# Optimization experiments

Hardware: AMD Instinct MI355X
Metric: run time of the kernel (lower is better)

Reference implementation:

```python
import jax, jax.numpy as jnp
import numpy as np

B, T, D, H = 2, 2048, 1024, 16
DH = D // H
PD = 6
SCALE = DH ** -0.5
_PAIRS4 = [(0, 1), (0, 2), (0, 3), (1, 2), (1, 3), (2, 3)]
_J6 = jnp.array([[0, 0, 0, 0, 0, 1], [0, 0, 0, 0, -1, 0], [0, 0, 0, 1, 0, 0],
                 [0, 0, 1, 0, 0, 0], [0, -1, 0, 0, 0, 0], [1, 0, 0, 0, 0, 0]], dtype=jnp.float32)


def exterior(p1, p2):
    # p1, p2: (..., 4) -> normalized 6-d Plucker line (..., 6)
    parts = [p1[..., i] * p2[..., j] - p1[..., j] * p2[..., i] for i, j in _PAIRS4]
    L = jnp.stack(parts, axis=-1)
    n = jnp.linalg.norm(L, axis=-1, keepdims=True)
    return L / jnp.clip(n, 1e-12)


def setup_inputs() -> dict:
    key = jax.random.key(0)
    ks = jax.random.split(key, 12)
    s = 0.02
    return {
        'x': jax.random.normal(ks[0], (B, T, D), jnp.float32),
        'qkv_w': jax.random.normal(ks[1], (D, 3 * D), jnp.float32) * s,
        'qkv_b': jnp.zeros((3 * D,), jnp.float32),
        'w1_write': jax.random.normal(ks[2], (D, 4 * H), jnp.float32) * s,
        'w2_write': jax.random.normal(ks[3], (D, 4 * H), jnp.float32) * s,
        'w1_read': jax.random.normal(ks[4], (D, 4 * H), jnp.float32) * s,
        'w2_read': jax.random.normal(ks[5], (D, 4 * H), jnp.float32) * s,
        'memv_w': jax.random.normal(ks[6], (D, D), jnp.float32) * s,
        'memv_b': jnp.zeros((D,), jnp.float32),
        'memg_w': jax.random.normal(ks[7], (D, H), jnp.float32) * s,
        'memg_b': jnp.zeros((H,), jnp.float32),
        'mem_scale': jnp.full((H,), 0.1, jnp.float32),
        'rw_mix': jnp.zeros((), jnp.float32),
        'out_w': jax.random.normal(ks[8], (D, D), jnp.float32) * s,
        'out_b': jnp.zeros((D,), jnp.float32),
        'decay_logits': jnp.full((H,), 4.6, jnp.float32),
    }


def reference(x, qkv_w, qkv_b, w1_write, w2_write, w1_read, w2_read,
              memv_w, memv_b, memg_w, memg_b, mem_scale, rw_mix,
              out_w, out_b, decay_logits):
    # ---- standard causal softmax attention ----
    qkv = (x @ qkv_w + qkv_b).reshape(B, T, 3, H, DH).transpose(2, 0, 3, 1, 4)
    q, k, v = qkv[0], qkv[1], qkv[2]                      # each (B,H,T,DH)
    scores = jnp.einsum('bhtd,bhsd->bhts', q, k) * SCALE
    mask = jnp.triu(jnp.ones((T, T), bool), 1)
    scores = jnp.where(mask[None, None], -jnp.inf, scores)
    attn = jax.nn.softmax(scores, axis=-1)                # dropout=0 (eval)
    seq_out = jnp.einsum('bhts,bhsd->bthd', attn, v).reshape(B, T, D)

    # ---- Plucker lines for write (prev->cur) and read ----
    x_prev = jnp.concatenate([jnp.zeros((B, 1, D), x.dtype), x[:, :-1]], axis=1)
    w1 = (x_prev @ w1_write).reshape(B, T, H, 4)
    w2 = (x @ w2_write).reshape(B, T, H, 4)
    write_lines = exterior(w1, w2)                        # (B,T,H,6)
    r1 = (x @ w1_read).reshape(B, T, H, 4)
    r2 = (x @ w2_read).reshape(B, T, H, 4)
    read_lines = exterior(r1, r2)

    Jw = jnp.einsum('bthi,ij->bhtj', write_lines, _J6)    # (B,H,T,6)
    Jr = jnp.einsum('bthi,ij->bhtj', read_lines, _J6)
    rd = read_lines.transpose(0, 2, 1, 3)                 # (B,H,T,6)

    # ---- decay-weighted cumsum of 6x6 outer-product states ----
    decays = jax.nn.sigmoid(decay_logits)                 # (H,)
    pos = jnp.arange(T, dtype=x.dtype)
    decay_inv = (1.0 / jnp.clip(decays, 1e-6))[:, None] ** pos[None]   # (H,T)
    decay_fwd = decays[:, None] ** pos[None]                           # (H,T)

    def shifted_state(Jv):
        outer = Jv[..., :, None] * Jv[..., None, :]       # (B,H,T,6,6)
        ow = outer * decay_inv[None, :, :, None, None]
        M = jnp.cumsum(ow, axis=2)
        M = jnp.concatenate([jnp.zeros((B, H, 1, PD, PD), x.dtype), M[:, :, :-1]], axis=2)
        return M * decay_fwd[None, :, :, None, None]

    Mw = shifted_state(Jw)
    Mr = shifted_state(Jr)

    score_w = jnp.einsum('bhti,bhtij,bhtj->bht', rd, Mw, rd)
    score_r = jnp.einsum('bhti,bhtij,bhtj->bht', Jw, Mr, Jw)
    alpha = jax.nn.sigmoid(rw_mix)
    mem_score = (1 - alpha) * score_w + alpha * score_r   # (B,H,T)

    mem_val = x @ memv_w + memv_b                         # (B,T,D)
    gate = jax.nn.sigmoid(x @ memg_w + memg_b)            # (B,T,H)
    mem_score_t = mem_score.transpose(0, 2, 1)            # (B,T,H)
    gated = jax.nn.sigmoid(mem_score_t * mem_scale[None, None, :]) * gate
    gated = gated.mean(axis=-1, keepdims=True)            # (B,T,1)

    return (seq_out + gated * mem_val) @ out_w + out_b
```

## Files before the change

### kernel.cpp

```cpp
#include <hip/hip_runtime.h>

#define Bb 2
#define Tt 2048
#define Dd 1024
#define Hh 16
#define LDC 4480

typedef __attribute__((ext_vector_type(8))) short s16x8;
typedef __attribute__((ext_vector_type(4))) float f32x4;
typedef __attribute__((ext_vector_type(8))) _Float16 f16x8;

__device__ __forceinline__ float bf2f(unsigned short u) {
  unsigned v = ((unsigned)u) << 16;
  union { unsigned u; float f; } c; c.u = v; return c.f;
}
__device__ __forceinline__ unsigned short f2bf(float f) {
  union { float f; unsigned u; } c; c.f = f;
  unsigned u = c.u + 0x7fffu + ((c.u >> 16) & 1u);
  return (unsigned short)(u >> 16);
}
__device__ __forceinline__ float sigm(float x) { return 1.f / (1.f + expf(-x)); }

typedef const __attribute__((address_space(1))) void* gas_ptr;
typedef __attribute__((address_space(3))) void* las_ptr;
__device__ __forceinline__ void gload_lds16(const unsigned short* g, unsigned short* l) {
  __builtin_amdgcn_global_load_lds((gas_ptr)g, (las_ptr)l, 16, 0, 0);
}



__global__ __launch_bounds__(256) void prep_kernel(const float* __restrict__ x,
                                                   const float* __restrict__ qkv_w,
                                                   const float* __restrict__ w1w,
                                                   const float* __restrict__ w2w,
                                                   const float* __restrict__ w1r,
                                                   const float* __restrict__ w2r,
                                                   const float* __restrict__ memg_w,
                                                   const float* __restrict__ memv_w,
                                                   const float* __restrict__ out_w,
                                                   const float* __restrict__ qkv_b,
                                                   const float* __restrict__ memg_b,
                                                   const float* __restrict__ memv_b,
                                                   unsigned short* __restrict__ xb,
                                                   unsigned short* __restrict__ WT,
                                                   unsigned short* __restrict__ outT,
                                                   float* __restrict__ biasC) {
  __shared__ float tile[32][33];
  int id = blockIdx.x;
  if (id < 2048) {
    int i = id * 256 + threadIdx.x;
    int row = i >> 7;
    int k8 = i & 127;
    const float4* xv = reinterpret_cast<const float4*>(x + (size_t)i * 8);
    float4 a = xv[0], b = xv[1];
    s16x8 out;
    out[0] = (short)f2bf(a.x); out[1] = (short)f2bf(a.y);
    out[2] = (short)f2bf(a.z); out[3] = (short)f2bf(a.w);
    out[4] = (short)f2bf(b.x); out[5] = (short)f2bf(b.y);
    out[6] = (short)f2bf(b.z); out[7] = (short)f2bf(b.w);
    int mt = row >> 4, kt = k8 >> 2, quad = k8 & 3;
    int lane = (row & 15) + quad * 16;
    *(s16x8*)&xb[(((size_t)mt * 32 + kt) * 64 + lane) * 8] = out;
  } else if (id < 6528) {
    int j = id - 2048;
    int n0 = (j % 140) * 32, kt = j / 140, k0 = kt * 32;
    int tx = threadIdx.x & 31, ty = threadIdx.x >> 5;
#pragma unroll
    for (int i = 0; i < 4; i++) {
      int k = k0 + ty + i * 8, n = n0 + tx;
      float v;
      if (n < 3072)       v = qkv_w[(size_t)k * 3072 + n];
      else if (n < 3136)  v = w1w[k * 64 + (n - 3072)];
      else if (n < 3200)  v = w2w[k * 64 + (n - 3136)];
      else if (n < 3264)  v = w1r[k * 64 + (n - 3200)];
      else if (n < 3328)  v = w2r[k * 64 + (n - 3264)];
      else if (n < 3344)  v = memg_w[k * 16 + (n - 3328)];
      else if (n < 3392)  v = 0.f;
      else if (n < 4416)  v = memv_w[(size_t)k * 1024 + (n - 3392)];
      else                v = 0.f;
      tile[ty + i * 8][tx] = v;
    }
    __syncthreads();
    if (threadIdx.x < 128) {
      int nl = threadIdx.x & 31, quad = threadIdx.x >> 5;
      s16x8 out;
#pragma unroll
      for (int e = 0; e < 8; e++) out[e] = (short)f2bf(tile[quad * 8 + e][nl]);
      int nt = (n0 >> 4) + (nl >> 4);
      int lane = (nl & 15) + quad * 16;
      *(s16x8*)&WT[(((size_t)nt * 32 + kt) * 64 + lane) * 8] = out;
    }
  } else if (id < 7552) {
    int j = id - 6528;
    int n0 = (j & 31) * 32, kt = j >> 5, k0 = kt * 32;
    int tx = threadIdx.x & 31, ty = threadIdx.x >> 5;
#pragma unroll
    for (int i = 0; i < 4; i++) {
      int k = k0 + ty + i * 8, n = n0 + tx;
      tile[ty + i * 8][tx] = out_w[(size_t)k * 1024 + n];
    }
    __syncthreads();
    if (threadIdx.x < 128) {
      int nl = threadIdx.x & 31, quad = threadIdx.x >> 5;
      s16x8 out;
#pragma unroll
      for (int e = 0; e < 8; e++) out[e] = (short)f2bf(tile[quad * 8 + e][nl]);
      int nt = (n0 >> 4) + (nl >> 4);
      int lane = (nl & 15) + quad * 16;
      *(s16x8*)&outT[(((size_t)nt * 32 + kt) * 64 + lane) * 8] = out;
    }
  } else {
    int i = (id - 7552) * 256 + threadIdx.x;
    if (i < LDC) {
      float v = 0.f;
      if (i < 3072) v = qkv_b[i];
      else if (i >= 3328 && i < 3344) v = memg_b[i - 3328];
      else if (i >= 3392 && i < 4416) v = memv_b[i - 3392];
      biasC[i] = v;
    }
  }
}


template <int MODE>
__global__ __launch_bounds__(256) void gemm_frag_kernel(const unsigned short* __restrict__ Af,
                                                        const unsigned short* __restrict__ Bf,
                                                        void* __restrict__ Cout,
                                                        const float* __restrict__ bias) {
  __shared__ __align__(16) unsigned short lds[2][16][512];
  int mTile, nTile;
  if (MODE == 0) {
    const int xx = blockIdx.x & 7, local = blockIdx.x >> 3;
    mTile = (xx >> 1) * 8 + (local & 7);
    nTile = (xx & 1) * 18 + (local >> 3);
    if (nTile >= 35) return;
  } else {
    mTile = blockIdx.x >> 3;
    nTile = blockIdx.x & 7;
  }
  const int lane = threadIdx.x & 63, wid = threadIdx.x >> 6;
  const int quad = lane >> 4, c16 = lane & 15;
  const int wm = wid >> 1, wn = wid & 1;
  const int mt0 = mTile * 8 + wm * 4;
  const int nt0 = nTile * 8 + wn * 4;

  const unsigned short* src[4];
#pragma unroll
  for (int i = 0; i < 4; i++) {
    int f = wid * 4 + i;
    src[i] = ((f < 8) ? (Af + (size_t)(mTile * 8 + f) * 16384)
                      : (Bf + (size_t)(nTile * 8 + (f - 8)) * 16384))
             + (size_t)lane * 8;
  }

  f32x4 acc[4][4] = {};

#pragma unroll
  for (int i = 0; i < 4; i++) gload_lds16(src[i], &lds[0][wid * 4 + i][0]);
  __syncthreads();

  int buf = 0;
  for (int kt = 0; kt < 32; kt++) {
    if (kt + 1 < 32) {
#pragma unroll
      for (int i = 0; i < 4; i++)
        gload_lds16(src[i] + (size_t)(kt + 1) * 512, &lds[buf ^ 1][wid * 4 + i][0]);
    }
    s16x8 a[4], b[4];
#pragma unroll
    for (int i = 0; i < 4; i++) {
      a[i] = *(const s16x8*)&lds[buf][wm * 4 + i][lane * 8];
      b[i] = *(const s16x8*)&lds[buf][8 + wn * 4 + i][lane * 8];
    }
#pragma unroll
    for (int mt = 0; mt < 4; mt++)
#pragma unroll
      for (int nt = 0; nt < 4; nt++)
        acc[mt][nt] = __builtin_amdgcn_mfma_f32_16x16x32_bf16(a[mt], b[nt],
                                                              acc[mt][nt], 0, 0, 0);
    __syncthreads();
    buf ^= 1;
  }

#pragma unroll
  for (int mt = 0; mt < 4; mt++)
#pragma unroll
    for (int nt = 0; nt < 4; nt++) {
      int col = (nt0 + nt) * 16 + c16;
      float bv = bias[col];
#pragma unroll
      for (int r = 0; r < 4; r++) {
        int row = (mt0 + mt) * 16 + quad * 4 + r;
        if (MODE == 0)
          ((unsigned short*)Cout)[(size_t)row * 4480 + col] = f2bf(acc[mt][nt][r] + bv);
        else
          ((float*)Cout)[(size_t)row * 1024 + col] = acc[mt][nt][r] + bv;
      }
    }
}


__device__ __forceinline__ void ext6(const float* p, const float* q, float* L) {
  L[0] = p[0] * q[1] - p[1] * q[0];
  L[1] = p[0] * q[2] - p[2] * q[0];
  L[2] = p[0] * q[3] - p[3] * q[0];
  L[3] = p[1] * q[2] - p[2] * q[1];
  L[4] = p[1] * q[3] - p[3] * q[1];
  L[5] = p[2] * q[3] - p[3] * q[2];
  float n = sqrtf(L[0]*L[0] + L[1]*L[1] + L[2]*L[2] + L[3]*L[3] + L[4]*L[4] + L[5]*L[5]);
  float inv = 1.f / fmaxf(n, 1e-12f);
#pragma unroll
  for (int k = 0; k < 6; k++) L[k] *= inv;
}


__global__ __launch_bounds__(256) void post1_kernel(const unsigned short* __restrict__ Cq,
                                                    unsigned short* __restrict__ Kt,
                                                    unsigned short* __restrict__ Vt,
                                                    float* __restrict__ Jw,
                                                    float* __restrict__ Jr,
                                                    float* __restrict__ rd) {
  __shared__ unsigned short vt[32 * 66];
  int id = blockIdx.x;
  int tid = threadIdx.x;
  if (id < 2048) {
    int kb = id & 63, bh = id >> 6;
    int b = bh >> 4, h = bh & 15;
    size_t tbase = ((size_t)bh * 64 + kb) * 2048;
    {
      int key = tid >> 3, p = tid & 7, dg = p ^ (key & 7);
      size_t src = (size_t)(b * Tt + kb * 32 + key) * LDC + 1024 + h * 64 + dg * 8;
      s16x8 kv = *(const s16x8*)&Cq[src];
      *(s16x8*)&Kt[tbase + (size_t)tid * 8] = kv;
    }
    {
      int row = tid >> 3, c = tid & 7;
      size_t src = (size_t)(b * Tt + kb * 32 + row) * LDC + 2048 + h * 64 + c * 8;
      s16x8 vv = *(const s16x8*)&Cq[src];
#pragma unroll
      for (int e = 0; e < 8; e++) {
        union { _Float16 hf; unsigned short s; } cv;
        cv.hf = (_Float16)bf2f((unsigned short)vv[e]);
        vt[row * 66 + c * 8 + e] = cv.s;
      }
    }
    __syncthreads();
    {
      int d = tid >> 2, p = tid & 3, cq = p ^ ((d >> 2) & 3);
      s16x8 out;
#pragma unroll
      for (int e = 0; e < 8; e++) {
        int key = ((e >> 2) & 1) * 16 + cq * 4 + (e & 3);
        out[e] = (short)vt[key * 66 + d];
      }
      *(s16x8*)&Vt[tbase + (size_t)tid * 8] = out;
    }
  } else {
    int idx = (id - 2048) * 256 + tid;
    int h = idx & 15, t = (idx >> 4) & 2047, b = idx >> 15;
    size_t row = (size_t)(b * Tt + t) * LDC;
    float w1[4], w2[4], r1[4], r2[4];
#pragma unroll
    for (int k = 0; k < 4; k++) {
      w1[k] = (t > 0) ? bf2f(Cq[row - LDC + 3072 + h * 4 + k]) : 0.f;
      w2[k] = bf2f(Cq[row + 3136 + h * 4 + k]);
      r1[k] = bf2f(Cq[row + 3200 + h * 4 + k]);
      r2[k] = bf2f(Cq[row + 3264 + h * 4 + k]);
    }
    float Lw[6], Lr[6];
    ext6(w1, w2, Lw);
    ext6(r1, r2, Lr);
    size_t ob = ((size_t)(b * Hh + h) * Tt + t) * 6;
    Jw[ob + 0] = Lw[5]; Jw[ob + 1] = -Lw[4]; Jw[ob + 2] = Lw[3];
    Jw[ob + 3] = Lw[2]; Jw[ob + 4] = -Lw[1]; Jw[ob + 5] = Lw[0];
    Jr[ob + 0] = Lr[5]; Jr[ob + 1] = -Lr[4]; Jr[ob + 2] = Lr[3];
    Jr[ob + 3] = Lr[2]; Jr[ob + 4] = -Lr[1]; Jr[ob + 5] = Lr[0];
#pragma unroll
    for (int k = 0; k < 6; k++) rd[ob + k] = Lr[k];
  }
}


__device__ __forceinline__ void do_tile(int ks, int q0, int quad, int c16,
                                        const s16x8& qf0, const s16x8& qf1,
                                        const s16x8 kf[2][2], const f16x8 vb[4],
                                        float& l_i, f32x4 o[4]) {
  f32x4 st0 = {}, st1 = {};
  __builtin_amdgcn_s_setprio(1);
  st0 = __builtin_amdgcn_mfma_f32_16x16x32_bf16(kf[0][0], qf0, st0, 0, 0, 0);
  st0 = __builtin_amdgcn_mfma_f32_16x16x32_bf16(kf[0][1], qf1, st0, 0, 0, 0);
  st1 = __builtin_amdgcn_mfma_f32_16x16x32_bf16(kf[1][0], qf0, st1, 0, 0, 0);
  st1 = __builtin_amdgcn_mfma_f32_16x16x32_bf16(kf[1][1], qf1, st1, 0, 0, 0);
  __builtin_amdgcn_s_setprio(0);
  bool need_mask = (ks + 31 > q0);
  f16x8 pa;
  float lp = 0.f;
#pragma unroll
  for (int r = 0; r < 4; r++) {
    float v0 = st0[r] * 0.125f;
    float v1 = st1[r] * 0.125f;
    if (need_mask) {
      v0 = (ks + quad * 4 + r      <= q0 + c16) ? v0 : -1e30f;
      v1 = (ks + 16 + quad * 4 + r <= q0 + c16) ? v1 : -1e30f;
    }
    float p0 = __expf(v0);
    float p1 = __expf(v1);
    lp += p0 + p1;
    pa[r]     = (_Float16)p0;
    pa[4 + r] = (_Float16)p1;
  }
  l_i += lp;
  __builtin_amdgcn_s_setprio(1);
#pragma unroll
  for (int nt = 0; nt < 4; nt++)
    o[nt] = __builtin_amdgcn_mfma_f32_16x16x32_f16(pa, vb[nt], o[nt], 0, 0, 0);
  __builtin_amdgcn_s_setprio(0);
}

__global__ __launch_bounds__(256) void attn_kernel(const unsigned short* __restrict__ Cq,
                                                   const unsigned short* __restrict__ Kt,
                                                   const unsigned short* __restrict__ Vt,
                                                   unsigned short* __restrict__ po) {
  const int id = blockIdx.x;
  const int xcd = id & 7, rest = id >> 3;
  const int g = rest & 15;
  const int bh = ((rest >> 4) << 3) | xcd;
  const int b = bh >> 4, h = bh & 15;
  const int w = threadIdx.x >> 6, lane = threadIdx.x & 63;
  const int quad = lane >> 4, c16 = lane & 15;
  const int pi = g * 4 + w;
  const int qA = pi * 16, qB = 2032 - pi * 16;
  const int nkA = qA + 16, nkB = 2048 - pi * 16;
  const char* Kbase = (const char*)(Kt + (size_t)bh * 64 * 2048);
  const char* Vbase = (const char*)(Vt + (size_t)bh * 64 * 2048);
  const int vK0 = c16 * 128 + ((quad       ^ (c16 & 7)) * 16);
  const int vK1 = c16 * 128 + (((4 + quad) ^ (c16 & 7)) * 16);
  const int vV  = c16 * 64  + ((quad ^ ((c16 >> 2) & 3)) * 16);

  size_t rowA = (size_t)(b * Tt + qA + c16) * LDC + h * 64;
  size_t rowB = (size_t)(b * Tt + qB + c16) * LDC + h * 64;
  s16x8 qA0 = *(const s16x8*)&Cq[rowA + quad * 8];
  s16x8 qA1 = *(const s16x8*)&Cq[rowA + 32 + quad * 8];
  s16x8 qB0 = *(const s16x8*)&Cq[rowB + quad * 8];
  s16x8 qB1 = *(const s16x8*)&Cq[rowB + 32 + quad * 8];

  float lA = 0.f, lB = 0.f;
  f32x4 oA[4] = {}, oB[4] = {};

  s16x8 kfX[2][2], kfY[2][2];
  f16x8 vbX[4], vbY[4];

#define LOADT(dstK, dstV, kb) do {                                   \
    const char* Kb_ = Kbase + (size_t)(kb) * 4096;                   \
    const char* Vb_ = Vbase + (size_t)(kb) * 4096;                   \
    dstK[0][0] = *(const s16x8*)(Kb_ + vK0);                         \
    dstK[0][1] = *(const s16x8*)(Kb_ + vK1);                         \
    dstK[1][0] = *(const s16x8*)(Kb_ + 2048 + vK0);                  \
    dstK[1][1] = *(const s16x8*)(Kb_ + 2048 + vK1);                  \
    dstV[0] = *(const f16x8*)(Vb_ + vV);                             \
    dstV[1] = *(const f16x8*)(Vb_ + 1024 + vV);                      \
    dstV[2] = *(const f16x8*)(Vb_ + 2048 + vV);                      \
    dstV[3] = *(const f16x8*)(Vb_ + 3072 + vV);                      \
  } while (0)

  LOADT(kfX, vbX, 0);
  for (int ks = 0; ks < nkB; ks += 64) {
    if (ks + 32 < nkB) LOADT(kfY, vbY, (ks >> 5) + 1);
    do_tile(ks, qB, quad, c16, qB0, qB1, kfX, vbX, lB, oB);
    if (ks < nkA)
      do_tile(ks, qA, quad, c16, qA0, qA1, kfX, vbX, lA, oA);
    if (ks + 32 < nkB) {
      if (ks + 64 < nkB) LOADT(kfX, vbX, (ks >> 5) + 2);
      do_tile(ks + 32, qB, quad, c16, qB0, qB1, kfY, vbY, lB, oB);
      if (ks + 32 < nkA)
        do_tile(ks + 32, qA, quad, c16, qA0, qA1, kfY, vbY, lA, oA);
    }
  }
#undef LOADT

  lB += __shfl_xor(lB, 16, 64); lB += __shfl_xor(lB, 32, 64);
  lA += __shfl_xor(lA, 16, 64); lA += __shfl_xor(lA, 32, 64);
  float invB = 1.f / lB, invA = 1.f / lA;
#pragma unroll
  for (int r = 0; r < 4; r++) {
    float ivB = __shfl(invB, quad * 4 + r, 64);
    float ivA = __shfl(invA, quad * 4 + r, 64);
    size_t baseB = (size_t)(b * Tt + qB + quad * 4 + r) * Dd + h * 64;
    size_t baseA = (size_t)(b * Tt + qA + quad * 4 + r) * Dd + h * 64;
#pragma unroll
    for (int nt = 0; nt < 4; nt++) {
      po[baseB + nt * 16 + c16] = f2bf(oB[nt][r] * ivB);
      po[baseA + nt * 16 + c16] = f2bf(oA[nt][r] * ivA);
    }
  }
}


__global__ __launch_bounds__(64) void scanA_kernel(const float* __restrict__ Jw,
                                                   const float* __restrict__ Jr,
                                                   const float* __restrict__ decay_logits,
                                                   float* __restrict__ chunkA) {
  int blk = blockIdx.x;
  int chunk = blk & 15, bh = (blk >> 4) & 31, type = blk >> 9;
  int lane = threadIdx.x;
  const float* V = (type == 0 ? Jw : Jr) + ((size_t)bh * Tt + chunk * 128) * 6;
  __shared__ float v[768];
  for (int i = lane; i < 768; i += 64) v[i] = V[i];
  __syncthreads();
  float d = sigm(decay_logits[bh & 15]);
  int ll = lane < 36 ? lane : 35;
  int i6 = ll / 6, j6 = ll % 6;
  float A = 0.f;
  for (int s = 0; s < 128; s++) A = d * A + v[s * 6 + i6] * v[s * 6 + j6];
  if (lane < 36) chunkA[((size_t)(type * 32 + bh) * 16 + chunk) * 36 + lane] = A;
}


__global__ __launch_bounds__(128) void scanB_kernel(const float* __restrict__ Jw,
                                                    const float* __restrict__ Jr,
                                                    const float* __restrict__ rd,
                                                    const float* __restrict__ chunkA,
                                                    const float* __restrict__ decay_logits,
                                                    float* __restrict__ score_w,
                                                    float* __restrict__ score_r) {
  int blk = blockIdx.x;
  int chunk = blk & 15, bh = (blk >> 4) & 31, type = blk >> 9;
  int tl = threadIdx.x;
  size_t tb = ((size_t)bh * Tt + chunk * 128) * 6;
  const float* U = (type == 0 ? rd : Jw) + tb;
  const float* W = (type == 0 ? Jw : Jr) + tb;
  __shared__ float wv[768];
  __shared__ float Bm[36];
  for (int i = tl; i < 768; i += 128) wv[i] = W[i];
  float d = sigm(decay_logits[bh & 15]);
  if (tl < 36) {
    float dS = powf(d, 128.f);
    float Bv = 0.f;
    size_t base = (size_t)(type * 32 + bh) * 16;
    for (int c = 0; c < chunk; c++)
      Bv = dS * Bv + d * chunkA[(base + c) * 36 + tl];
    Bm[tl] = Bv;
  }
  __syncthreads();
  float u[6];
#pragma unroll
  for (int i = 0; i < 6; i++) u[i] = U[tl * 6 + i];
  float q = 0.f;
#pragma unroll
  for (int i = 0; i < 6; i++) {
    float bi = 0.f;
#pragma unroll
    for (int j = 0; j < 6; j++) bi += Bm[i * 6 + j] * u[j];
    q += u[i] * bi;
  }
  float acc = 0.f;
  for (int s = 0; s < tl; s++) {
    const float* ws = &wv[s * 6];
    float dot = u[0]*ws[0] + u[1]*ws[1] + u[2]*ws[2] + u[3]*ws[3] + u[4]*ws[4] + u[5]*ws[5];
    acc = d * (acc + dot * dot);
  }
  float score = acc + powf(d, (float)tl) * q;
  float* outp = (type == 0 ? score_w : score_r);
  outp[(size_t)bh * Tt + chunk * 128 + tl] = score;
}


__global__ __launch_bounds__(256) void combine_kernel(const unsigned short* __restrict__ po,
                                                      const unsigned short* __restrict__ Cq,
                                                      const float* __restrict__ score_w,
                                                      const float* __restrict__ score_r,
                                                      const float* __restrict__ mem_scale,
                                                      const float* __restrict__ rw_mix,
                                                      unsigned short* __restrict__ fused) {
  __shared__ float tmp[16];
  int rowi = blockIdx.x;
  int b = rowi >> 11, t = rowi & 2047;
  float alpha = sigm(rw_mix[0]);
  if (threadIdx.x < 16) {
    int h = threadIdx.x;
    size_t sh = (size_t)(b * 16 + h) * Tt + t;
    float ms = (1.f - alpha) * score_w[sh] + alpha * score_r[sh];
    float gate = sigm(bf2f(Cq[(size_t)rowi * LDC + 3328 + h]));
    tmp[h] = sigm(ms * mem_scale[h]) * gate;
  }
  __syncthreads();
  float g = 0.f;
#pragma unroll
  for (int h = 0; h < 16; h++) g += tmp[h];
  g *= (1.f / 16.f);
  if (threadIdx.x < 128) {
    int c = threadIdx.x;
    int d0 = c * 8;
    s16x8 ov = *(const s16x8*)&po[((size_t)b * Tt + t) * Dd + d0];
    s16x8 mv = *(const s16x8*)&Cq[(size_t)rowi * LDC + 3392 + d0];
    s16x8 out;
#pragma unroll
    for (int e = 0; e < 8; e++)
      out[e] = (short)f2bf(bf2f((unsigned short)ov[e]) + g * bf2f((unsigned short)mv[e]));
    int mt = rowi >> 4, kt = c >> 2, quad = c & 3;
    int lane = (rowi & 15) + quad * 16;
    *(s16x8*)&fused[(((size_t)mt * 32 + kt) * 64 + lane) * 8] = out;
  }
}


extern "C" void kernel_launch(void* const* d_in, const int* in_sizes, int n_in,
                              void* d_out, int out_size, void* d_ws, size_t ws_size,
                              hipStream_t stream) {
  (void)in_sizes; (void)n_in; (void)out_size; (void)ws_size;
  const float* x         = (const float*)d_in[0];
  const float* qkv_w     = (const float*)d_in[1];
  const float* qkv_b     = (const float*)d_in[2];
  const float* w1w       = (const float*)d_in[3];
  const float* w2w       = (const float*)d_in[4];
  const float* w1r       = (const float*)d_in[5];
  const float* w2r       = (const float*)d_in[6];
  const float* memv_w    = (const float*)d_in[7];
  const float* memv_b    = (const float*)d_in[8];
  const float* memg_w    = (const float*)d_in[9];
  const float* memg_b    = (const float*)d_in[10];
  const float* mem_scale = (const float*)d_in[11];
  const float* rw_mix    = (const float*)d_in[12];
  const float* out_w     = (const float*)d_in[13];
  const float* out_b     = (const float*)d_in[14];
  const float* decay_l   = (const float*)d_in[15];

  char* w = (char*)d_ws;
  unsigned short* xb    = (unsigned short*)(w + 0);
  unsigned short* Kt    = (unsigned short*)(w + 0);
  unsigned short* WT    = (unsigned short*)(w + 8388608);
  unsigned short* Vt    = (unsigned short*)(w + 8388608);
  unsigned short* outT  = (unsigned short*)(w + 17563648);
  float*          biasC = (float*)(w + 19660800);
  unsigned short* Cbuf  = (unsigned short*)(w + 19678720);
  unsigned short* po    = (unsigned short*)(w + 56378880);
  float*          Jw    = (float*)(w + 73680384);
  float*          Jr    = (float*)(w + 75253248);
  float*          rd    = (float*)(w + 76826112);
  float*          chA   = (float*)(w + 78398976);
  float*          sw    = (float*)(w + 78693888);
  float*          sr    = (float*)(w + 78956032);
  unsigned short* fused = (unsigned short*)(w + 79218176);

  prep_kernel<<<7570, 256, 0, stream>>>(x, qkv_w, w1w, w2w, w1r, w2r, memg_w, memv_w,
                                        out_w, qkv_b, memg_b, memv_b,
                                        xb, WT, outT, biasC);

  gemm_frag_kernel<0><<<1152, 256, 0, stream>>>(xb, WT, Cbuf, biasC);

  post1_kernel<<<2304, 256, 0, stream>>>(Cbuf, Kt, Vt, Jw, Jr, rd);
  attn_kernel<<<512, 256, 0, stream>>>(Cbuf, Kt, Vt, po);
  scanA_kernel<<<1024, 64, 0, stream>>>(Jw, Jr, decay_l, chA);
  scanB_kernel<<<1024, 128, 0, stream>>>(Jw, Jr, rd, chA, decay_l, sw, sr);
  combine_kernel<<<4096, 256, 0, stream>>>(po, Cbuf, sw, sr, mem_scale, rw_mix, fused);

  gemm_frag_kernel<1><<<256, 256, 0, stream>>>(fused, outT, d_out, out_b);
}
```

Baseline: 271.0 us.

## Split attention key range across two waves per query pair and merge via LDS

The attention kernel now assigns each paired query block (A and B) to a 128-thread block whose two waves split the key tiles roughly evenly, then merges partial outputs and row sums through shared memory. This quadruples the grid, which shortens the per-wave serial loop and gives better load balance. Separately, the softmax scale is folded into K during the transpose kernel, removing a multiply per score. Folding the scale adds a bf16 rounding of the scaled K. The merge relies on there being no running max, since the kernel uses unnormalized exp sums.

Measured after the change: 281.5 us. 1.04x slower.

```diff
diff --git a/kernel.cpp b/kernel.cpp
--- a/kernel.cpp
+++ b/kernel.cpp
@@ -231,7 +231,11 @@
       int key = tid >> 3, p = tid & 7, dg = p ^ (key & 7);
       size_t src = (size_t)(b * Tt + kb * 32 + key) * LDC + 1024 + h * 64 + dg * 8;
       s16x8 kv = *(const s16x8*)&Cq[src];
-      *(s16x8*)&Kt[tbase + (size_t)tid * 8] = kv;
+      s16x8 kvs;
+#pragma unroll
+      for (int e = 0; e < 8; e++)
+        kvs[e] = (short)f2bf(bf2f((unsigned short)kv[e]) * 0.125f);
+      *(s16x8*)&Kt[tbase + (size_t)tid * 8] = kvs;
     }
     {
       int row = tid >> 3, c = tid & 7;
@@ -297,8 +301,8 @@
   float lp = 0.f;
 #pragma unroll
   for (int r = 0; r < 4; r++) {
-    float v0 = st0[r] * 0.125f;
-    float v1 = st1[r] * 0.125f;
+    float v0 = st0[r];
+    float v1 = st1[r];
     if (need_mask) {
       v0 = (ks + quad * 4 + r      <= q0 + c16) ? v0 : -1e30f;
       v1 = (ks + 16 + quad * 4 + r <= q0 + c16) ? v1 : -1e30f;
@@ -317,20 +321,24 @@
   __builtin_amdgcn_s_setprio(0);
 }
 
-__global__ __launch_bounds__(256) void attn_kernel(const unsigned short* __restrict__ Cq,
+__global__ __launch_bounds__(128) void attn_kernel(const unsigned short* __restrict__ Cq,
                                                    const unsigned short* __restrict__ Kt,
                                                    const unsigned short* __restrict__ Vt,
                                                    unsigned short* __restrict__ po) {
+  __shared__ float mrg[64][35];
   const int id = blockIdx.x;
   const int xcd = id & 7, rest = id >> 3;
-  const int g = rest & 15;
-  const int bh = ((rest >> 4) << 3) | xcd;
+  const int pi = rest & 63;
+  const int bh = ((rest >> 6) << 3) | xcd;
   const int b = bh >> 4, h = bh & 15;
-  const int w = threadIdx.x >> 6, lane = threadIdx.x & 63;
+  const int kw = threadIdx.x >> 6, lane = threadIdx.x & 63;
   const int quad = lane >> 4, c16 = lane & 15;
-  const int pi = g * 4 + w;
   const int qA = pi * 16, qB = 2032 - pi * 16;
   const int nkA = qA + 16, nkB = 2048 - pi * 16;
+  const int TA = (nkA + 31) >> 5, TB = (nkB + 31) >> 5;
+  const int ht = (TA >= 16) ? 16 : (32 - TA);
+  const int t0 = kw ? ht : 0;
+  const int t1 = kw ? TB : ht;
   const char* Kbase = (const char*)(Kt + (size_t)bh * 64 * 2048);
   const char* Vbase = (const char*)(Vt + (size_t)bh * 64 * 2048);
   const int vK0 = c16 * 128 + ((quad       ^ (c16 & 7)) * 16);
@@ -363,20 +371,47 @@
     dstV[3] = *(const f16x8*)(Vb_ + 3072 + vV);                      \
   } while (0)
 
-  LOADT(kfX, vbX, 0);
-  for (int ks = 0; ks < nkB; ks += 64) {
-    if (ks + 32 < nkB) LOADT(kfY, vbY, (ks >> 5) + 1);
-    do_tile(ks, qB, quad, c16, qB0, qB1, kfX, vbX, lB, oB);
-    if (ks < nkA)
-      do_tile(ks, qA, quad, c16, qA0, qA1, kfX, vbX, lA, oA);
-    if (ks + 32 < nkB) {
-      if (ks + 64 < nkB) LOADT(kfX, vbX, (ks >> 5) + 2);
-      do_tile(ks + 32, qB, quad, c16, qB0, qB1, kfY, vbY, lB, oB);
-      if (ks + 32 < nkA)
-        do_tile(ks + 32, qA, quad, c16, qA0, qA1, kfY, vbY, lA, oA);
+  LOADT(kfX, vbX, t0);
+  for (int t = t0; t < t1; t += 2) {
+    if (t + 1 < t1) LOADT(kfY, vbY, t + 1);
+    {
+      int ks = t * 32;
+      do_tile(ks, qB, quad, c16, qB0, qB1, kfX, vbX, lB, oB);
+      if (ks < nkA)
+        do_tile(ks, qA, quad, c16, qA0, qA1, kfX, vbX, lA, oA);
+    }
+    if (t + 1 < t1) {
+      if (t + 2 < t1) LOADT(kfX, vbX, t + 2);
+      int ks = (t + 1) * 32;
+      do_tile(ks, qB, quad, c16, qB0, qB1, kfY, vbY, lB, oB);
+      if (ks < nkA)
+        do_tile(ks, qA, quad, c16, qA0, qA1, kfY, vbY, lA, oA);
     }
   }
 #undef LOADT
+
+  if (kw == 1) {
+#pragma unroll
+    for (int nt = 0; nt < 4; nt++)
+#pragma unroll
+      for (int r = 0; r < 4; r++) {
+        mrg[lane][nt * 4 + r]      = oB[nt][r];
+        mrg[lane][16 + nt * 4 + r] = oA[nt][r];
+      }
+    mrg[lane][32] = lB;
+    mrg[lane][33] = lA;
+  }
+  __syncthreads();
+  if (kw == 1) return;
+#pragma unroll
+  for (int nt = 0; nt < 4; nt++)
+#pragma unroll
+    for (int r = 0; r < 4; r++) {
+      oB[nt][r] += mrg[lane][nt * 4 + r];
+      oA[nt][r] += mrg[lane][16 + nt * 4 + r];
+    }
+  lB += mrg[lane][32];
+  lA += mrg[lane][33];
 
   lB += __shfl_xor(lB, 16, 64); lB += __shfl_xor(lB, 32, 64);
   lA += __shfl_xor(lA, 16, 64); lA += __shfl_xor(lA, 32, 64);
@@ -549,7 +584,7 @@
   gemm_frag_kernel<0><<<1152, 256, 0, stream>>>(xb, WT, Cbuf, biasC);
 
   post1_kernel<<<2304, 256, 0, stream>>>(Cbuf, Kt, Vt, Jw, Jr, rd);
-  attn_kernel<<<512, 256, 0, stream>>>(Cbuf, Kt, Vt, po);
+  attn_kernel<<<2048, 128, 0, stream>>>(Cbuf, Kt, Vt, po);
   scanA_kernel<<<1024, 64, 0, stream>>>(Jw, Jr, decay_l, chA);
   scanB_kernel<<<1024, 128, 0, stream>>>(Jw, Jr, rd, chA, decay_l, sw, sr);
   combine_kernel<<<4096, 256, 0, stream>>>(po, Cbuf, sw, sr, mem_scale, rw_mix, fused);
```
